# Performance work log

Measured on AMD Instinct MI355X. Metric: run time of the kernel, lower is better.

Reference implementation:

```python
import jax, jax.numpy as jnp
import numpy as np

H = 4  # num_heads


def transformer_conv(x, src, dst, wq, bq, wk, bk, wv, bv, ws, bs):
    # PyG TransformerConv, concat=False, root_weight=True, eval mode (no dropout).
    N = x.shape[0]
    C = wq.shape[1] // H  # per-head channels
    q = (x @ wq + bq).reshape(N, H, C)
    k = (x @ wk + bk).reshape(N, H, C)
    v = (x @ wv + bv).reshape(N, H, C)
    # per-edge attention logits: query at dst, key at src
    logits = (q[dst] * k[src]).sum(-1) / jnp.sqrt(jnp.asarray(C, x.dtype))  # [E,H]
    # scatter-softmax over incoming edges of each destination node
    m = jax.lax.stop_gradient(jax.ops.segment_max(logits, dst, num_segments=N))
    m = jnp.where(jnp.isfinite(m), m, jnp.zeros_like(m))
    e = jnp.exp(logits - m[dst])
    denom = jax.ops.segment_sum(e, dst, num_segments=N)
    alpha = e / (denom[dst] + 1e-16)  # [E,H]
    out = jax.ops.segment_sum(alpha[:, :, None] * v[src], dst, num_segments=N)  # [N,H,C]
    return out.mean(axis=1) + x @ ws + bs  # head-average + skip


def setup_inputs() -> dict:
    key = jax.random.key(0)
    ks = jax.random.split(key, 16)
    N, E, D, HID, OUT = 50000, 800000, 128, 32, 40
    s = 0.05
    inp = {
        "x": jax.random.normal(ks[0], (N, D), jnp.float32),
        "edge_index": jax.random.randint(ks[1], (2, E), 0, N, jnp.int64),
        "wq1": jax.random.normal(ks[2], (D, H * HID), jnp.float32) * s,
        "bq1": jnp.zeros((H * HID,), jnp.float32),
        "wk1": jax.random.normal(ks[3], (D, H * HID), jnp.float32) * s,
        "bk1": jnp.zeros((H * HID,), jnp.float32),
        "wv1": jax.random.normal(ks[4], (D, H * HID), jnp.float32) * s,
        "bv1": jnp.zeros((H * HID,), jnp.float32),
        "ws1": jax.random.normal(ks[5], (D, HID), jnp.float32) * s,
        "bs1": jnp.zeros((HID,), jnp.float32),
        "wq2": jax.random.normal(ks[6], (HID, H * HID), jnp.float32) * s,
        "bq2": jnp.zeros((H * HID,), jnp.float32),
        "wk2": jax.random.normal(ks[7], (HID, H * HID), jnp.float32) * s,
        "bk2": jnp.zeros((H * HID,), jnp.float32),
        "wv2": jax.random.normal(ks[8], (HID, H * HID), jnp.float32) * s,
        "bv2": jnp.zeros((H * HID,), jnp.float32),
        "ws2": jax.random.normal(ks[9], (HID, HID), jnp.float32) * s,
        "bs2": jnp.zeros((HID,), jnp.float32),
        "wc": jax.random.normal(ks[10], (HID, OUT), jnp.float32) * s,
        "bc": jnp.zeros((OUT,), jnp.float32),
    }
    return inp


def reference(x, edge_index, wq1, bq1, wk1, bk1, wv1, bv1, ws1, bs1,
              wq2, bq2, wk2, bk2, wv2, bv2, ws2, bs2, wc, bc):
    src, dst = edge_index[0], edge_index[1]
    h = jax.nn.relu(transformer_conv(x, src, dst, wq1, bq1, wk1, bk1, wv1, bv1, ws1, bs1))
    h = jax.nn.relu(transformer_conv(h, src, dst, wq2, bq2, wk2, bk2, wv2, bv2, ws2, bs2))
    return h @ wc + bc
```

## Files before the change

### kernel.cpp

```cpp
#include <hip/hip_runtime.h>
#include <hip/hip_bf16.h>

typedef __attribute__((ext_vector_type(8))) short short8;
typedef __attribute__((ext_vector_type(4))) float floatx4;
typedef __attribute__((ext_vector_type(4))) unsigned short ushort4v;

__device__ inline unsigned short f2bf(float x) {
    unsigned int u = __float_as_uint(x);
    u += 0x7FFFu + ((u >> 16) & 1u);
    return (unsigned short)(u >> 16);
}
__device__ inline float bf2f(unsigned short h) {
    return __uint_as_float(((unsigned int)h) << 16);
}
__device__ inline float blo(unsigned int u) { return __uint_as_float(u << 16); }
__device__ inline float bhi(unsigned int u) { return __uint_as_float(u & 0xFFFF0000u); }

__global__ __launch_bounds__(256) void hist_kernel(
    const int* __restrict__ dst, int* __restrict__ deg, int E)
{
    int e = blockIdx.x * blockDim.x + threadIdx.x;
    if (e < E) atomicAdd(&deg[dst[e]], 1);
}

__global__ __launch_bounds__(256) void scan_part(
    const int* __restrict__ deg, int* __restrict__ bsum, int N)
{
    __shared__ int ws[4];
    const int base = blockIdx.x * 1024;
    const int tid = threadIdx.x, lane = tid & 63, w = tid >> 6;
    int s = 0;
#pragma unroll
    for (int j = 0; j < 4; j++) {
        int i = base + j * 256 + tid;
        if (i < N) s += deg[i];
    }
#pragma unroll
    for (int off = 1; off < 64; off <<= 1) s += __shfl_xor(s, off, 64);
    if (lane == 0) ws[w] = s;
    __syncthreads();
    if (tid == 0) bsum[blockIdx.x] = ws[0] + ws[1] + ws[2] + ws[3];
}

__global__ __launch_bounds__(64) void scan_tops(
    const int* __restrict__ bsum, int* __restrict__ boff,
    int* __restrict__ rowptr, int nb, int N)
{
    int lane = threadIdx.x;
    int v = (lane < nb) ? bsum[lane] : 0;
    int inc = v;
#pragma unroll
    for (int off = 1; off < 64; off <<= 1) {
        int t = __shfl_up(inc, off, 64);
        if (lane >= off) inc += t;
    }
    if (lane < nb) boff[lane] = inc - v;
    if (lane == 63) rowptr[N] = inc;
}

__global__ __launch_bounds__(256) void scan_final(
    const int* __restrict__ deg, const int* __restrict__ boff,
    int* __restrict__ rowptr, int* __restrict__ cursor, int N)
{
    __shared__ int woff[4];
    const int base = blockIdx.x * 1024;
    const int tid = threadIdx.x, lane = tid & 63, w = tid >> 6;
    const int i0 = base + tid * 4;
    int v0 = (i0     < N) ? deg[i0]     : 0;
    int v1 = (i0 + 1 < N) ? deg[i0 + 1] : 0;
    int v2 = (i0 + 2 < N) ? deg[i0 + 2] : 0;
    int v3 = (i0 + 3 < N) ? deg[i0 + 3] : 0;
    int ts = v0 + v1 + v2 + v3;
    int inc = ts;
#pragma unroll
    for (int off = 1; off < 64; off <<= 1) {
        int t = __shfl_up(inc, off, 64);
        if (lane >= off) inc += t;
    }
    if (lane == 63) woff[w] = inc;
    __syncthreads();
    int wpre = 0;
    if (w > 0) wpre += woff[0];
    if (w > 1) wpre += woff[1];
    if (w > 2) wpre += woff[2];
    int exc = boff[blockIdx.x] + wpre + inc - ts;
    int p0 = exc, p1 = exc + v0, p2 = p1 + v1, p3 = p2 + v2;
    if (i0     < N) { rowptr[i0]     = p0; cursor[i0]     = p0; }
    if (i0 + 1 < N) { rowptr[i0 + 1] = p1; cursor[i0 + 1] = p1; }
    if (i0 + 2 < N) { rowptr[i0 + 2] = p2; cursor[i0 + 2] = p2; }
    if (i0 + 3 < N) { rowptr[i0 + 3] = p3; cursor[i0 + 3] = p3; }
}

__global__ __launch_bounds__(256) void fill_kernel(
    const int* __restrict__ src, const int* __restrict__ dst,
    int* __restrict__ cursor, int* __restrict__ perm, int E)
{
    int e = blockIdx.x * blockDim.x + threadIdx.x;
    if (e >= E) return;
    int pos = atomicAdd(&cursor[dst[e]], 1);
    perm[pos] = src[e];
}

__global__ __launch_bounds__(128) void wprep_all(
    const float* __restrict__ wq1, const float* __restrict__ bq1,
    const float* __restrict__ wk1, const float* __restrict__ bk1,
    const float* __restrict__ wv1, const float* __restrict__ bv1,
    const float* __restrict__ ws1, const float* __restrict__ bs1,
    const float* __restrict__ wq2, const float* __restrict__ bq2,
    const float* __restrict__ wk2, const float* __restrict__ bk2,
    const float* __restrict__ wv2, const float* __restrict__ bv2,
    const float* __restrict__ ws2, const float* __restrict__ bs2,
    unsigned short* __restrict__ wt1h, unsigned short* __restrict__ wt1l,
    float* __restrict__ bias1,
    unsigned short* __restrict__ wt2h, unsigned short* __restrict__ wt2l,
    float* __restrict__ bias2)
{
    const int layer = (blockIdx.x >= 416) ? 1 : 0;
    const int c = blockIdx.x - layer * 416;
    const int t = threadIdx.x;
    const int L = layer ? 32 : 128;
    if (t >= L) return;
    const float* w; const float* b; int cc, ncols;
    if (c < 384) {
        int m = c >> 7; cc = c & 127; ncols = 128;
        if (layer == 0) {
            w = (m == 0) ? wq1 : ((m == 1) ? wk1 : wv1);
            b = (m == 0) ? bq1 : ((m == 1) ? bk1 : bv1);
        } else {
            w = (m == 0) ? wq2 : ((m == 1) ? wk2 : wv2);
            b = (m == 0) ? bq2 : ((m == 1) ? bk2 : bv2);
        }
    } else {
        cc = c - 384; ncols = 32;
        w = layer ? ws2 : ws1; b = layer ? bs2 : bs1;
    }
    unsigned short* wh = layer ? wt2h : wt1h;
    unsigned short* wl = layer ? wt2l : wt1l;
    float* bias = layer ? bias2 : bias1;
    float val = w[t * ncols + cc];
    unsigned short h = f2bf(val);
    wh[c * L + t] = h;
    wl[c * L + t] = f2bf(val - bf2f(h));
    if (t == 0) bias[c] = b[cc];
}

template <int L>
__global__ __launch_bounds__(256) void proj_mfma(
    const float* __restrict__ xin,
    const unsigned short* __restrict__ wt_hi,
    const unsigned short* __restrict__ wt_lo,
    const float* __restrict__ bias,
    float* __restrict__ q, unsigned short* __restrict__ kvp,
    float* __restrict__ skip, int N)
{
    constexpr int LP = L + 8;
    constexpr int KS = L / 32;
    constexpr int SI = (32 * (L / 4)) / 256;
    __shared__ unsigned short xh[2][32 * LP];
    __shared__ unsigned short xl[2][32 * LP];
    __shared__ float scr[4][32 * 36];
    const int tid = threadIdx.x, lane = tid & 63, w = tid >> 6;
    const int li = lane & 15, quad = lane >> 4;
    const int slot = __builtin_amdgcn_readfirstlane(blockIdx.y * 4 + w);
    const bool hasT = slot < 13;

    int t0 = 24, t1 = 25;
    if (slot < 4)       { t0 = slot * 2; t1 = t0 + 1; }
    else if (slot < 12) { t0 = 4 + slot; t1 = 12 + slot; }

    short8 Ah[2][KS], Al[2][KS];
    float bias_r[2][4];
    if (hasT) {
#pragma unroll
        for (int ti = 0; ti < 2; ti++) {
            int tt = ti ? t1 : t0;
#pragma unroll
            for (int ks = 0; ks < KS; ks++) {
                long off = (long)(tt * 16 + li) * L + ks * 32 + quad * 8;
                Ah[ti][ks] = *(const short8*)(wt_hi + off);
                Al[ti][ks] = *(const short8*)(wt_lo + off);
            }
#pragma unroll
            for (int r = 0; r < 4; r++)
                bias_r[ti][r] = bias[tt * 16 + quad * 4 + r];
        }
    }

    const int nb0 = blockIdx.x * 256;
    float* myscr = scr[w];
    unsigned int* su = (unsigned int*)myscr;

    float4 xv[SI];
    auto issue_loads = [&](int c) {
#pragma unroll
        for (int s = 0; s < SI; s++) {
            int f = s * 256 + tid;
            int row = f / (L / 4), c4 = (f - row * (L / 4)) * 4;
            int n = nb0 + c * 32 + row;
            xv[s] = (n < N) ? *(const float4*)(xin + (long)n * L + c4)
                            : make_float4(0.f, 0.f, 0.f, 0.f);
        }
    };
    auto cvt_store = [&](int buf) {
#pragma unroll
        for (int s = 0; s < SI; s++) {
            int f = s * 256 + tid;
            int row = f / (L / 4), c4 = (f - row * (L / 4)) * 4;
            unsigned short h0 = f2bf(xv[s].x), h1 = f2bf(xv[s].y),
                           h2 = f2bf(xv[s].z), h3 = f2bf(xv[s].w);
            ushort4v hs = {h0, h1, h2, h3};
            ushort4v ls = {f2bf(xv[s].x - bf2f(h0)), f2bf(xv[s].y - bf2f(h1)),
                           f2bf(xv[s].z - bf2f(h2)), f2bf(xv[s].w - bf2f(h3))};
            *(ushort4v*)(xh[buf] + row * LP + c4) = hs;
            *(ushort4v*)(xl[buf] + row * LP + c4) = ls;
        }
    };

    issue_loads(0);
    cvt_store(0);
    __syncthreads();

    for (int c = 0; c < 8; c++) {
        if (c < 7) issue_loads(c + 1);
        const int n0c = nb0 + c * 32;
        if (hasT) {
            const int buf = c & 1;
#pragma unroll
            for (int half = 0; half < 2; half++) {
                short8 Bh[KS], Bl[KS];
#pragma unroll
                for (int ks = 0; ks < KS; ks++) {
                    int off = (half * 16 + li) * LP + ks * 32 + quad * 8;
                    Bh[ks] = *(const short8*)(xh[buf] + off);
                    Bl[ks] = *(const short8*)(xl[buf] + off);
                }
                floatx4 accv[2];
#pragma unroll
                for (int ti = 0; ti < 2; ti++) {
                    floatx4 acc = {0.f, 0.f, 0.f, 0.f};
#pragma unroll
                    for (int ks = 0; ks < KS; ks++) {
                        acc = __builtin_amdgcn_mfma_f32_16x16x32_bf16(Ah[ti][ks], Bh[ks], acc, 0, 0, 0);
                        acc = __builtin_amdgcn_mfma_f32_16x16x32_bf16(Ah[ti][ks], Bl[ks], acc, 0, 0, 0);
                        acc = __builtin_amdgcn_mfma_f32_16x16x32_bf16(Al[ti][ks], Bh[ks], acc, 0, 0, 0);
                    }
#pragma unroll
                    for (int r = 0; r < 4; r++) acc[r] += bias_r[ti][r];
                    accv[ti] = acc;
                }
                const int row = half * 16 + li;
                if (slot < 4 || slot == 12) {
                    *(floatx4*)(myscr + row * 36 + quad * 4)      = accv[0];
                    *(floatx4*)(myscr + row * 36 + 16 + quad * 4) = accv[1];
                } else {
                    unsigned int k01 = (unsigned int)f2bf(accv[0][0]) | ((unsigned int)f2bf(accv[0][1]) << 16);
                    unsigned int k23 = (unsigned int)f2bf(accv[0][2]) | ((unsigned int)f2bf(accv[0][3]) << 16);
                    unsigned int v01 = (unsigned int)f2bf(accv[1][0]) | ((unsigned int)f2bf(accv[1][1]) << 16);
                    unsigned int v23 = (unsigned int)f2bf(accv[1][2]) | ((unsigned int)f2bf(accv[1][3]) << 16);
                    uint4 pk = make_uint4(k01, v01, k23, v23);
                    *(uint4*)(su + row * 20 + quad * 4) = pk;
                }
            }
            if (slot < 4) {
#pragma unroll
                for (int it = 0; it < 4; it++) {
                    int idx = it * 64 + lane;
                    int nl = idx >> 3, seg = idx & 7;
                    int node = n0c + nl;
                    if (node < N) {
                        floatx4 vv = *(floatx4*)(myscr + nl * 36 + seg * 4);
                        *(floatx4*)(q + (long)node * 128 + slot * 32 + seg * 4) = vv;
                    }
                }
            } else if (slot == 12) {
#pragma unroll
                for (int it = 0; it < 4; it++) {
                    int idx = it * 64 + lane;
                    int nl = idx >> 3, seg = idx & 7;
                    int node = n0c + nl;
                    if (node < N) {
                        floatx4 vv = *(floatx4*)(myscr + nl * 36 + seg * 4);
                        *(floatx4*)(skip + (long)node * 32 + seg * 4) = vv;
                    }
                }
            } else {
                const int i = slot - 4;
#pragma unroll
                for (int it = 0; it < 2; it++) {
                    int idx = it * 64 + lane;
                    int nl = idx >> 2, part = idx & 3;
                    int node = n0c + nl;
                    if (node < N) {
                        uint4 vv = *(uint4*)(su + nl * 20 + part * 4);
                        *(uint4*)((unsigned int*)(kvp + (long)node * 256) + i * 16 + part * 4) = vv;
                    }
                }
            }
        }
        __syncthreads();
        if (c < 7) cvt_store((c + 1) & 1);
        __syncthreads();
    }
}

__global__ __launch_bounds__(256) void attn_kernel(
    const float* __restrict__ q, const unsigned short* __restrict__ kvp,
    const int* __restrict__ rowptr, const int* __restrict__ perm,
    const float* __restrict__ skip, float* __restrict__ h, int N)
{
    const int wid = (blockIdx.x * 256 + threadIdx.x) >> 6;
    const int lane = threadIdx.x & 63;
    if (wid >= N) return;
    const int d = __builtin_amdgcn_readfirstlane(wid);
    const int eh = lane >> 5;
    const int sl = lane & 31;
    const int hh = sl >> 3;
    const int g  = sl & 7;
    const int dimoff = hh * 64 + g * 8;
    const float4 q4 = *(const float4*)(q + (long)d * 128 + hh * 32 + g * 4);
    const int beg = rowptr[d], end = rowptr[d + 1];
    const int n = end - beg;
    const int na = (n + 1) >> 1;
    const int my_off = beg + (eh ? na : 0);
    const int my_cnt = eh ? (n - na) : na;
    const float scale = 0.17677669529663687f;
    float m = -INFINITY, den = 0.f;
    float o0 = 0.f, o1 = 0.f, o2 = 0.f, o3 = 0.f;
    for (int j = 0; j < na; j += 2) {
        const bool ok0 = j < my_cnt, ok1 = (j + 1) < my_cnt;
        const int i0 = ok0 ? (my_off + j) : beg;
        const int i1 = ok1 ? (my_off + j + 1) : beg;
        const int s0 = perm[i0], s1 = perm[i1];
        const uint4 a0 = *(const uint4*)(kvp + (long)s0 * 256 + dimoff);
        const uint4 a1 = *(const uint4*)(kvp + (long)s1 * 256 + dimoff);
        float p0 = q4.x * blo(a0.x) + q4.y * bhi(a0.x) + q4.z * blo(a0.z) + q4.w * bhi(a0.z);
        float p1 = q4.x * blo(a1.x) + q4.y * bhi(a1.x) + q4.z * blo(a1.z) + q4.w * bhi(a1.z);
        p0 += __shfl_xor(p0, 1);  p1 += __shfl_xor(p1, 1);
        p0 += __shfl_xor(p0, 2);  p1 += __shfl_xor(p1, 2);
        p0 += __shfl_xor(p0, 4);  p1 += __shfl_xor(p1, 4);
        const float l0 = ok0 ? p0 * scale : -INFINITY;
        const float l1 = ok1 ? p1 * scale : -INFINITY;
        const float nm = fmaxf(fmaxf(m, fmaxf(l0, l1)), -1e30f);
        const float sc = __expf(m - nm);
        const float w0 = __expf(l0 - nm);
        const float w1 = __expf(l1 - nm);
        den = den * sc + w0 + w1;
        o0 = o0 * sc + w0 * blo(a0.y) + w1 * blo(a1.y);
        o1 = o1 * sc + w0 * bhi(a0.y) + w1 * bhi(a1.y);
        o2 = o2 * sc + w0 * blo(a0.w) + w1 * blo(a1.w);
        o3 = o3 * sc + w0 * bhi(a0.w) + w1 * bhi(a1.w);
        m = nm;
    }
    {
        const float mo = __shfl_xor(m, 32);
        const float dn = __shfl_xor(den, 32);
        const float b0 = __shfl_xor(o0, 32);
        const float b1 = __shfl_xor(o1, 32);
        const float b2 = __shfl_xor(o2, 32);
        const float b3 = __shfl_xor(o3, 32);
        const float nm = fmaxf(fmaxf(m, mo), -1e30f);
        const float sa = __expf(m - nm);
        const float sb = __expf(mo - nm);
        den = den * sa + dn * sb;
        o0 = o0 * sa + b0 * sb;
        o1 = o1 * sa + b1 * sb;
        o2 = o2 * sa + b2 * sb;
        o3 = o3 * sa + b3 * sb;
    }
    const float inv = 1.f / (den + 1e-16f);
    o0 *= inv; o1 *= inv; o2 *= inv; o3 *= inv;
    o0 += __shfl_xor(o0, 8);  o1 += __shfl_xor(o1, 8);
    o2 += __shfl_xor(o2, 8);  o3 += __shfl_xor(o3, 8);
    o0 += __shfl_xor(o0, 16); o1 += __shfl_xor(o1, 16);
    o2 += __shfl_xor(o2, 16); o3 += __shfl_xor(o3, 16);
    if (lane < 8) {
        float4 sk = *(const float4*)(skip + (long)d * 32 + g * 4);
        float r0 = 0.25f * o0 + sk.x;
        float r1 = 0.25f * o1 + sk.y;
        float r2 = 0.25f * o2 + sk.z;
        float r3 = 0.25f * o3 + sk.w;
        r0 = r0 > 0.f ? r0 : 0.f;
        r1 = r1 > 0.f ? r1 : 0.f;
        r2 = r2 > 0.f ? r2 : 0.f;
        r3 = r3 > 0.f ? r3 : 0.f;
        *(float4*)(h + (long)d * 32 + g * 4) = make_float4(r0, r1, r2, r3);
    }
}

__global__ __launch_bounds__(256) void classify_kernel(
    const float* __restrict__ h, const float* __restrict__ wc,
    const float* __restrict__ bc, float* __restrict__ out, int N)
{
    int gid = blockIdx.x * blockDim.x + threadIdx.x;
    if (gid >= N * 40) return;
    int n = gid / 40, o = gid - (gid / 40) * 40;
    float acc = bc[o];
    const float* hr = h + (long)n * 32;
#pragma unroll
    for (int l = 0; l < 32; ++l) acc += hr[l] * wc[l * 40 + o];
    out[gid] = acc;
}

extern "C" void kernel_launch(void* const* d_in, const int* in_sizes, int n_in,
                              void* d_out, int out_size, void* d_ws, size_t ws_size,
                              hipStream_t stream)
{
    const float* x   = (const float*)d_in[0];
    const int* ei    = (const int*)d_in[1];
    const float* wq1 = (const float*)d_in[2];  const float* bq1 = (const float*)d_in[3];
    const float* wk1 = (const float*)d_in[4];  const float* bk1 = (const float*)d_in[5];
    const float* wv1 = (const float*)d_in[6];  const float* bv1 = (const float*)d_in[7];
    const float* ws1 = (const float*)d_in[8];  const float* bs1 = (const float*)d_in[9];
    const float* wq2 = (const float*)d_in[10]; const float* bq2 = (const float*)d_in[11];
    const float* wk2 = (const float*)d_in[12]; const float* bk2 = (const float*)d_in[13];
    const float* wv2 = (const float*)d_in[14]; const float* bv2 = (const float*)d_in[15];
    const float* ws2 = (const float*)d_in[16]; const float* bs2 = (const float*)d_in[17];
    const float* wc  = (const float*)d_in[18]; const float* bc  = (const float*)d_in[19];

    const int N = in_sizes[0] / 128;
    const int E = in_sizes[1] / 2;
    const int* src = ei;
    const int* dst = ei + E;

    char* p = (char*)d_ws;
    auto take = [&](size_t bytes) { char* r = p; p += (bytes + 255) & ~(size_t)255; return r; };
    float* q             = (float*)take((size_t)N * 128 * 4);
    unsigned short* kvp  = (unsigned short*)take((size_t)N * 256 * 2);
    float* skip          = (float*)take((size_t)N * 32 * 4);
    float* h1            = (float*)take((size_t)N * 32 * 4);
    float* h2            = (float*)take((size_t)N * 32 * 4);
    unsigned short* wt1h = (unsigned short*)take(416 * 128 * 2);
    unsigned short* wt1l = (unsigned short*)take(416 * 128 * 2);
    unsigned short* wt2h = (unsigned short*)take(416 * 32 * 2);
    unsigned short* wt2l = (unsigned short*)take(416 * 32 * 2);
    float* bias1         = (float*)take(416 * 4);
    float* bias2         = (float*)take(416 * 4);
    int* deg             = (int*)take((size_t)N * 4);
    int* rowptr          = (int*)take((size_t)(N + 1) * 4);
    int* cursor          = (int*)take((size_t)N * 4);
    int* perm            = (int*)take((size_t)E * 4);
    int* bsum            = (int*)take(64 * 4);
    int* boff            = (int*)take(64 * 4);

    const dim3 projGrid((N + 255) / 256, 4);
    const int eGrid    = (E + 255) / 256;
    const int attnGrid = (N + 3) / 4;
    const int nb       = (N + 1023) / 1024;

    wprep_all<<<832, 128, 0, stream>>>(wq1, bq1, wk1, bk1, wv1, bv1, ws1, bs1,
                                       wq2, bq2, wk2, bk2, wv2, bv2, ws2, bs2,
                                       wt1h, wt1l, bias1, wt2h, wt2l, bias2);
    hipMemsetAsync(deg, 0, (size_t)N * 4, stream);
    hist_kernel<<<eGrid, 256, 0, stream>>>(dst, deg, E);
    scan_part<<<nb, 256, 0, stream>>>(deg, bsum, N);
    scan_tops<<<1, 64, 0, stream>>>(bsum, boff, rowptr, nb, N);
    scan_final<<<nb, 256, 0, stream>>>(deg, boff, rowptr, cursor, N);
    fill_kernel<<<eGrid, 256, 0, stream>>>(src, dst, cursor, perm, E);

    proj_mfma<128><<<projGrid, 256, 0, stream>>>(x, wt1h, wt1l, bias1, q, kvp, skip, N);
    attn_kernel<<<attnGrid, 256, 0, stream>>>(q, kvp, rowptr, perm, skip, h1, N);

    proj_mfma<32><<<projGrid, 256, 0, stream>>>(h1, wt2h, wt2l, bias2, q, kvp, skip, N);
    attn_kernel<<<attnGrid, 256, 0, stream>>>(q, kvp, rowptr, perm, skip, h2, N);

    classify_kernel<<<(N * 40 + 255) / 256, 256, 0, stream>>>(h2, wc, bc, (float*)d_out, N);
}
```

Before: 379.5 us.

## Software-pipeline attention edge loop and fuse classifier into second attention

```diff
diff --git a/kernel.cpp b/kernel.cpp
--- a/kernel.cpp
+++ b/kernel.cpp
@@ -303,12 +303,17 @@
     }
 }
 
+template <bool FUSE_CLS>
 __global__ __launch_bounds__(256) void attn_kernel(
     const float* __restrict__ q, const unsigned short* __restrict__ kvp,
     const int* __restrict__ rowptr, const int* __restrict__ perm,
-    const float* __restrict__ skip, float* __restrict__ h, int N)
-{
+    const float* __restrict__ skip, float* __restrict__ h,
+    const float* __restrict__ wc, const float* __restrict__ bc,
+    float* __restrict__ out, int N, int E)
+{
+    __shared__ float hrow[4][32];
     const int wid = (blockIdx.x * 256 + threadIdx.x) >> 6;
+    const int wv = (threadIdx.x >> 6) & 3;
     const int lane = threadIdx.x & 63;
     if (wid >= N) return;
     const int d = __builtin_amdgcn_readfirstlane(wid);
@@ -326,31 +331,56 @@
     const float scale = 0.17677669529663687f;
     float m = -INFINITY, den = 0.f;
     float o0 = 0.f, o1 = 0.f, o2 = 0.f, o3 = 0.f;
-    for (int j = 0; j < na; j += 2) {
-        const bool ok0 = j < my_cnt, ok1 = (j + 1) < my_cnt;
-        const int i0 = ok0 ? (my_off + j) : beg;
-        const int i1 = ok1 ? (my_off + j + 1) : beg;
-        const int s0 = perm[i0], s1 = perm[i1];
-        const uint4 a0 = *(const uint4*)(kvp + (long)s0 * 256 + dimoff);
-        const uint4 a1 = *(const uint4*)(kvp + (long)s1 * 256 + dimoff);
-        float p0 = q4.x * blo(a0.x) + q4.y * bhi(a0.x) + q4.z * blo(a0.z) + q4.w * bhi(a0.z);
-        float p1 = q4.x * blo(a1.x) + q4.y * bhi(a1.x) + q4.z * blo(a1.z) + q4.w * bhi(a1.z);
-        p0 += __shfl_xor(p0, 1);  p1 += __shfl_xor(p1, 1);
-        p0 += __shfl_xor(p0, 2);  p1 += __shfl_xor(p1, 2);
-        p0 += __shfl_xor(p0, 4);  p1 += __shfl_xor(p1, 4);
-        const float l0 = ok0 ? p0 * scale : -INFINITY;
-        const float l1 = ok1 ? p1 * scale : -INFINITY;
-        const float nm = fmaxf(fmaxf(m, fmaxf(l0, l1)), -1e30f);
+
+    auto eidx = [&](int j) -> int {
+        int i = (j < my_cnt) ? (my_off + j) : beg;
+        return (i < E) ? i : 0;
+    };
+
+    int P0 = perm[eidx(4)], P1 = perm[eidx(5)], P2 = perm[eidx(6)], P3 = perm[eidx(7)];
+    uint4 A0, A1, A2, A3;
+    {
+        int s0 = perm[eidx(0)], s1 = perm[eidx(1)], s2 = perm[eidx(2)], s3 = perm[eidx(3)];
+        A0 = *(const uint4*)(kvp + (long)s0 * 256 + dimoff);
+        A1 = *(const uint4*)(kvp + (long)s1 * 256 + dimoff);
+        A2 = *(const uint4*)(kvp + (long)s2 * 256 + dimoff);
+        A3 = *(const uint4*)(kvp + (long)s3 * 256 + dimoff);
+    }
+
+    for (int j = 0; j < na; j += 4) {
+        uint4 B0 = *(const uint4*)(kvp + (long)P0 * 256 + dimoff);
+        uint4 B1 = *(const uint4*)(kvp + (long)P1 * 256 + dimoff);
+        uint4 B2 = *(const uint4*)(kvp + (long)P2 * 256 + dimoff);
+        uint4 B3 = *(const uint4*)(kvp + (long)P3 * 256 + dimoff);
+        int NP0 = perm[eidx(j + 8)],  NP1 = perm[eidx(j + 9)];
+        int NP2 = perm[eidx(j + 10)], NP3 = perm[eidx(j + 11)];
+
+        float p0 = q4.x * blo(A0.x) + q4.y * bhi(A0.x) + q4.z * blo(A0.z) + q4.w * bhi(A0.z);
+        float p1 = q4.x * blo(A1.x) + q4.y * bhi(A1.x) + q4.z * blo(A1.z) + q4.w * bhi(A1.z);
+        float p2 = q4.x * blo(A2.x) + q4.y * bhi(A2.x) + q4.z * blo(A2.z) + q4.w * bhi(A2.z);
+        float p3 = q4.x * blo(A3.x) + q4.y * bhi(A3.x) + q4.z * blo(A3.z) + q4.w * bhi(A3.z);
+        p0 += __shfl_xor(p0, 1);  p1 += __shfl_xor(p1, 1);  p2 += __shfl_xor(p2, 1);  p3 += __shfl_xor(p3, 1);
+        p0 += __shfl_xor(p0, 2);  p1 += __shfl_xor(p1, 2);  p2 += __shfl_xor(p2, 2);  p3 += __shfl_xor(p3, 2);
+        p0 += __shfl_xor(p0, 4);  p1 += __shfl_xor(p1, 4);  p2 += __shfl_xor(p2, 4);  p3 += __shfl_xor(p3, 4);
+        const float l0 = (j + 0 < my_cnt) ? p0 * scale : -INFINITY;
+        const float l1 = (j + 1 < my_cnt) ? p1 * scale : -INFINITY;
+        const float l2 = (j + 2 < my_cnt) ? p2 * scale : -INFINITY;
+        const float l3 = (j + 3 < my_cnt) ? p3 * scale : -INFINITY;
+        const float mb = fmaxf(fmaxf(l0, l1), fmaxf(l2, l3));
+        const float nm = fmaxf(fmaxf(m, mb), -1e30f);
         const float sc = __expf(m - nm);
-        const float w0 = __expf(l0 - nm);
-        const float w1 = __expf(l1 - nm);
-        den = den * sc + w0 + w1;
-        o0 = o0 * sc + w0 * blo(a0.y) + w1 * blo(a1.y);
-        o1 = o1 * sc + w0 * bhi(a0.y) + w1 * bhi(a1.y);
-        o2 = o2 * sc + w0 * blo(a0.w) + w1 * blo(a1.w);
-        o3 = o3 * sc + w0 * bhi(a0.w) + w1 * bhi(a1.w);
+        const float w0 = __expf(l0 - nm), w1 = __expf(l1 - nm);
+        const float w2 = __expf(l2 - nm), w3 = __expf(l3 - nm);
+        den = den * sc + ((w0 + w1) + (w2 + w3));
+        o0 = o0 * sc + w0 * blo(A0.y) + w1 * blo(A1.y) + w2 * blo(A2.y) + w3 * blo(A3.y);
+        o1 = o1 * sc + w0 * bhi(A0.y) + w1 * bhi(A1.y) + w2 * bhi(A2.y) + w3 * bhi(A3.y);
+        o2 = o2 * sc + w0 * blo(A0.w) + w1 * blo(A1.w) + w2 * blo(A2.w) + w3 * blo(A3.w);
+        o3 = o3 * sc + w0 * bhi(A0.w) + w1 * bhi(A1.w) + w2 * bhi(A2.w) + w3 * bhi(A3.w);
         m = nm;
-    }
+        A0 = B0; A1 = B1; A2 = B2; A3 = B3;
+        P0 = NP0; P1 = NP1; P2 = NP2; P3 = NP3;
+    }
+
     {
         const float mo = __shfl_xor(m, 32);
         const float dn = __shfl_xor(den, 32);
@@ -373,6 +403,7 @@
     o2 += __shfl_xor(o2, 8);  o3 += __shfl_xor(o3, 8);
     o0 += __shfl_xor(o0, 16); o1 += __shfl_xor(o1, 16);
     o2 += __shfl_xor(o2, 16); o3 += __shfl_xor(o3, 16);
+
     if (lane < 8) {
         float4 sk = *(const float4*)(skip + (long)d * 32 + g * 4);
         float r0 = 0.25f * o0 + sk.x;
@@ -383,22 +414,22 @@
         r1 = r1 > 0.f ? r1 : 0.f;
         r2 = r2 > 0.f ? r2 : 0.f;
         r3 = r3 > 0.f ? r3 : 0.f;
-        *(float4*)(h + (long)d * 32 + g * 4) = make_float4(r0, r1, r2, r3);
-    }
-}
-
-__global__ __launch_bounds__(256) void classify_kernel(
-    const float* __restrict__ h, const float* __restrict__ wc,
-    const float* __restrict__ bc, float* __restrict__ out, int N)
-{
-    int gid = blockIdx.x * blockDim.x + threadIdx.x;
-    if (gid >= N * 40) return;
-    int n = gid / 40, o = gid - (gid / 40) * 40;
-    float acc = bc[o];
-    const float* hr = h + (long)n * 32;
-#pragma unroll
-    for (int l = 0; l < 32; ++l) acc += hr[l] * wc[l * 40 + o];
-    out[gid] = acc;
+        if (FUSE_CLS) {
+            *(float4*)&hrow[wv][g * 4] = make_float4(r0, r1, r2, r3);
+        } else {
+            *(float4*)(h + (long)d * 32 + g * 4) = make_float4(r0, r1, r2, r3);
+        }
+    }
+    if (FUSE_CLS) {
+        __builtin_amdgcn_wave_barrier();
+        if (lane < 40) {
+            float acc = bc[lane];
+#pragma unroll
+            for (int l = 0; l < 32; ++l)
+                acc = fmaf(hrow[wv][l], wc[l * 40 + lane], acc);
+            out[(long)d * 40 + lane] = acc;
+        }
+    }
 }
 
 extern "C" void kernel_launch(void* const* d_in, const int* in_sizes, int n_in,
@@ -428,7 +459,6 @@
     unsigned short* kvp  = (unsigned short*)take((size_t)N * 256 * 2);
     float* skip          = (float*)take((size_t)N * 32 * 4);
     float* h1            = (float*)take((size_t)N * 32 * 4);
-    float* h2            = (float*)take((size_t)N * 32 * 4);
     unsigned short* wt1h = (unsigned short*)take(416 * 128 * 2);
     unsigned short* wt1l = (unsigned short*)take(416 * 128 * 2);
     unsigned short* wt2h = (unsigned short*)take(416 * 32 * 2);
@@ -458,10 +488,10 @@
     fill_kernel<<<eGrid, 256, 0, stream>>>(src, dst, cursor, perm, E);
 
     proj_mfma<128><<<projGrid, 256, 0, stream>>>(x, wt1h, wt1l, bias1, q, kvp, skip, N);
-    attn_kernel<<<attnGrid, 256, 0, stream>>>(q, kvp, rowptr, perm, skip, h1, N);
+    attn_kernel<false><<<attnGrid, 256, 0, stream>>>(q, kvp, rowptr, perm, skip, h1,
+                                                     wc, bc, (float*)d_out, N, E);
 
     proj_mfma<32><<<projGrid, 256, 0, stream>>>(h1, wt2h, wt2l, bias2, q, kvp, skip, N);
-    attn_kernel<<<attnGrid, 256, 0, stream>>>(q, kvp, rowptr, perm, skip, h2, N);
-
-    classify_kernel<<<(N * 40 + 255) / 256, 256, 0, stream>>>(h2, wc, bc, (float*)d_out, N);
-}
+    attn_kernel<true><<<attnGrid, 256, 0, stream>>>(q, kvp, rowptr, perm, skip, h1,
+                                                    wc, bc, (float*)d_out, N, E);
+}
```

Measured after the change: 360.0 us. -5.1%, faster.
